# Performance work log

Hardware: AMD Instinct MI355X
Metric: run time of the kernel (lower is better)

Reference implementation:

```python
import jax, jax.numpy as jnp
import numpy as np

NUM_BANDS = 30
SPLIT_FREQ = 30
M_PARAM = 1
DIM = 2048
BATCH = 16384


def _dct_mat(N):
    # Orthonormal DCT-II matrix D: dct(x) = x @ D.T, idct(y) = y @ D
    n = np.arange(N, dtype=np.float64)
    kk = n[:, None]
    M = np.cos(np.pi * (n + 0.5) * kk / N)
    s = np.full(N, np.sqrt(2.0 / N))
    s[0] = np.sqrt(1.0 / N)
    return jnp.asarray((M * s[:, None]).astype(np.float32))


def _band_scale(freq_weights, k, N):
    # Precompute the per-frequency scale vector the torch loop applies band-by-band.
    pts = np.linspace(0, N - 1, NUM_BANDS + 1).astype(np.int64)  # torch .long() truncation
    scale = jnp.ones((N,), dtype=freq_weights.dtype)
    for i in range(NUM_BANDS):
        s, e = int(pts[i]), int(pts[i + 1])
        if e <= SPLIT_FREQ:
            f = 1.0 + freq_weights[i] * k * (1.0 - i / NUM_BANDS)
        else:
            f = 1.0 - freq_weights[i] * k * (1.0 - (i - NUM_BANDS // M_PARAM) / NUM_BANDS)
        scale = scale.at[s:e].set(f)  # bands are disjoint; base is 1
    return scale


def setup_inputs() -> dict:
    key = jax.random.key(0)
    ks = jax.random.split(key, 6)
    g = 0.02  # small init like xavier_uniform with gain 0.5
    return {
        "x": jax.random.normal(ks[0], (BATCH, DIM), dtype=jnp.float32),
        "freq_weights": jnp.ones((NUM_BANDS,), dtype=jnp.float32),
        "k": jnp.float32(0.3),
        "W1": jax.random.normal(ks[1], (1024, DIM), dtype=jnp.float32) * g,
        "b1": jnp.zeros((1024,), dtype=jnp.float32),
        "W2": jax.random.normal(ks[2], (512, 1024), dtype=jnp.float32) * g,
        "b2": jnp.zeros((512,), dtype=jnp.float32),
        "Wmu": jax.random.normal(ks[3], (256, 512), dtype=jnp.float32) * g,
        "bmu": jnp.zeros((256,), dtype=jnp.float32),
        "Wlv": jax.random.normal(ks[4], (256, 512), dtype=jnp.float32) * g,
        "blv": jnp.zeros((256,), dtype=jnp.float32),
    }


def reference(x, freq_weights, k, W1, b1, W2, b2, Wmu, bmu, Wlv, blv):
    N = x.shape[-1]
    D = _dct_mat(N)
    # DCT -> per-band reweight -> IDCT, fused as two matmuls and one vector multiply
    xd = (x @ D.T) * _band_scale(freq_weights, k, N)
    xe = xd @ D
    h = jax.nn.relu(xe @ W1.T + b1)
    h = jax.nn.relu(h @ W2.T + b2)
    mu = h @ Wmu.T + bmu
    logvar = h @ Wlv.T + blv
    return (mu, logvar)
```

## Files before the change

kernel.cpp:

```cpp
#include <hip/hip_runtime.h>
#include <hip/hip_bf16.h>
#include <math.h>

#define DIM 2048
#define BATCH 16384

typedef __attribute__((ext_vector_type(8))) short short8;
typedef __attribute__((ext_vector_type(4))) float floatx4;
typedef unsigned short ushort_t;
typedef unsigned int uint_t;

__device__ __forceinline__ ushort_t f2bf(float f) {
    union { float f; unsigned u; } v; v.f = f;
    unsigned r = v.u + 0x7FFFu + ((v.u >> 16) & 1u);
    return (ushort_t)(r >> 16);
}

__device__ __forceinline__ uint_t cvt2bf(float a, float b) {
    __hip_bfloat162 h = __float22bfloat162_rn(float2{a, b});
    union { __hip_bfloat162 h; uint_t u; } v; v.h = h;
    return v.u;
}

__global__ void k_scale(const float* __restrict__ fw, const float* __restrict__ kp,
                        float* __restrict__ s) {
    int n = blockIdx.x * blockDim.x + threadIdx.x;
    if (n >= DIM) return;
    float kv = kp[0];
    float f = 1.0f;
    for (int i = 0; i < 30; ++i) {
        long s0 = (long)((double)i       * (double)(DIM - 1) / 30.0);
        long e0 = (long)((double)(i + 1) * (double)(DIM - 1) / 30.0);
        if (n >= s0 && n < e0) {
            if (e0 <= 30)
                f = 1.0f + fw[i] * kv * (1.0f - (float)i / 30.0f);
            else
                f = 1.0f - fw[i] * kv * (1.0f - (float)(i - 30) / 30.0f);
        }
    }
    s[n] = f;
}

__global__ void k_gen_d(ushort_t* __restrict__ D, ushort_t* __restrict__ Dt) {
    int idx = blockIdx.x * blockDim.x + threadIdx.x;
    int r = idx >> 11;
    int c = idx & (DIM - 1);
    const float w  = 7.6699039394282058e-4f;
    const float s0 = 0.02209708691207961f;
    const float s1 = 0.03125f;
    int m1 = ((2 * c + 1) * r) & (4 * DIM - 1);
    int m2 = ((2 * r + 1) * c) & (4 * DIM - 1);
    float v1 = cosf(w * (float)m1) * (r == 0 ? s0 : s1);
    float v2 = cosf(w * (float)m2) * (c == 0 ? s0 : s1);
    D[idx]  = f2bf(v1);
    Dt[idx] = f2bf(v2);
}

#define U_W1   262144
#define U_W2    65536
#define U_WH    16384
__global__ void k_cast_w(const float* __restrict__ W1, const float* __restrict__ W2,
                         const float* __restrict__ Wmu, const float* __restrict__ Wlv,
                         ushort_t* __restrict__ W1bf, ushort_t* __restrict__ W2bf,
                         ushort_t* __restrict__ Wcat) {
    int i = blockIdx.x * blockDim.x + threadIdx.x;
    const float* src; ushort_t* dst; int u;
    if (i < U_W1)                    { src = W1;  dst = W1bf;             u = i; }
    else if (i < U_W1 + U_W2)        { src = W2;  dst = W2bf;             u = i - U_W1; }
    else if (i < U_W1 + U_W2 + U_WH) { src = Wmu; dst = Wcat;             u = i - U_W1 - U_W2; }
    else                             { src = Wlv; dst = Wcat + 8 * U_WH;  u = i - U_W1 - U_W2 - U_WH; }
    const float4* p = reinterpret_cast<const float4*>(src) + 2 * (size_t)u;
    float4 a = p[0], b = p[1];
    short8 r;
    r[0] = (short)f2bf(a.x); r[1] = (short)f2bf(a.y);
    r[2] = (short)f2bf(a.z); r[3] = (short)f2bf(a.w);
    r[4] = (short)f2bf(b.x); r[5] = (short)f2bf(b.y);
    r[6] = (short)f2bf(b.z); r[7] = (short)f2bf(b.w);
    *reinterpret_cast<short8*>(dst + 8 * (size_t)u) = r;
}

template<int TM, int TN, int EPI, bool AF32>
__device__ __forceinline__ void gemm_core(
        const ushort_t* __restrict__ A, const float* __restrict__ Af,
        const ushort_t* __restrict__ B,
        ushort_t* __restrict__ Cb, float* __restrict__ Cf,
        const float* __restrict__ ep0, const float* __restrict__ ep1,
        int M, int N, int K) {
    constexpr int BM = 32 * TM;
    constexpr int BN = 32 * TN;
    __shared__ __align__(16) ushort_t As[BM * 32];
    __shared__ __align__(16) ushort_t Bs[BN * 32];

    const int tid  = threadIdx.x;
    const int lane = tid & 63;
    const int wave = tid >> 6;
    const int wm   = wave >> 1;
    const int wn   = wave & 1;
    const int q    = lane >> 4;
    const int l16  = lane & 15;

    const int tilesM = M / BM;
    const int tilesN = N / BN;
    const int bid = (int)blockIdx.x;
    const int xcd = bid & 7;
    const int j   = bid >> 3;
    const int bm  = xcd * (tilesM >> 3) + j / tilesN;
    const int bn  = j % tilesN;

    floatx4 acc[TM][TN];
    #pragma unroll
    for (int i = 0; i < TM; ++i)
        #pragma unroll
        for (int jj = 0; jj < TN; ++jj)
            acc[i][jj] = (floatx4){0.f, 0.f, 0.f, 0.f};

    const long aBase = (long)bm * BM * K;
    const long bBase = (long)bn * BN * K;

    float4 pf[4];
    const float* abase = nullptr;
    if constexpr (AF32) {
        abase = Af + aBase + (long)(tid >> 3) * K + (tid & 7) * 4;
        #pragma unroll
        for (int i = 0; i < 4; ++i)
            pf[i] = *reinterpret_cast<const float4*>(abase + (long)i * 32 * K);
    }

    for (int kt = 0; kt < K; kt += 32) {
        __syncthreads();
        if constexpr (AF32) {
            const int rowb = tid >> 3, fseg = tid & 7;
            #pragma unroll
            for (int i = 0; i < 4; ++i) {
                int row  = rowb + i * 32;
                int lseg = (fseg >> 1) ^ ((row >> 1) & 3);
                uint2 w;
                w.x = cvt2bf(pf[i].x, pf[i].y);
                w.y = cvt2bf(pf[i].z, pf[i].w);
                *reinterpret_cast<uint2*>(As + row * 32 + lseg * 8 + (fseg & 1) * 4) = w;
            }
        } else {
            #pragma unroll
            for (int i = 0; i < BM / 64; ++i) {
                int idx = tid + i * 256;
                int row = idx >> 2, seg = idx & 3;
                int gseg = seg ^ ((row >> 1) & 3);
                const ushort_t* g = A + aBase + (long)row * K + kt + gseg * 8;
                __builtin_amdgcn_global_load_lds(
                    (const __attribute__((address_space(1))) void*)g,
                    (__attribute__((address_space(3))) void*)(As + idx * 8),
                    16, 0, 0);
            }
        }
        #pragma unroll
        for (int i = 0; i < BN / 64; ++i) {
            int idx = tid + i * 256;
            int row = idx >> 2, seg = idx & 3;
            int gseg = seg ^ ((row >> 1) & 3);
            const ushort_t* g = B + bBase + (long)row * K + kt + gseg * 8;
            __builtin_amdgcn_global_load_lds(
                (const __attribute__((address_space(1))) void*)g,
                (__attribute__((address_space(3))) void*)(Bs + idx * 8),
                16, 0, 0);
        }
        __syncthreads();

        short8 af[TM], bfr[TN];
        #pragma unroll
        for (int t = 0; t < TM; ++t) {
            int srow = wm * TM * 16 + t * 16 + l16;
            int rseg = q ^ ((srow >> 1) & 3);
            af[t] = *reinterpret_cast<const short8*>(&As[srow * 32 + rseg * 8]);
        }
        #pragma unroll
        for (int t = 0; t < TN; ++t) {
            int srow = wn * TN * 16 + t * 16 + l16;
            int rseg = q ^ ((srow >> 1) & 3);
            bfr[t] = *reinterpret_cast<const short8*>(&Bs[srow * 32 + rseg * 8]);
        }
        if constexpr (AF32) {
            if (kt + 32 < K) {
                const float* ab = abase + kt + 32;
                #pragma unroll
                for (int i = 0; i < 4; ++i)
                    pf[i] = *reinterpret_cast<const float4*>(ab + (long)i * 32 * K);
            }
        }
        #pragma unroll
        for (int i = 0; i < TM; ++i)
            #pragma unroll
            for (int jj = 0; jj < TN; ++jj)
                acc[i][jj] = __builtin_amdgcn_mfma_f32_16x16x32_bf16(
                    af[i], bfr[jj], acc[i][jj], 0, 0, 0);
    }

    #pragma unroll
    for (int i = 0; i < TM; ++i) {
        #pragma unroll
        for (int jj = 0; jj < TN; ++jj) {
            #pragma unroll
            for (int r = 0; r < 4; ++r) {
                int row = bm * BM + wm * TM * 16 + i * 16 + q * 4 + r;
                int col = bn * BN + wn * TN * 16 + jj * 16 + l16;
                float v = acc[i][jj][r];
                if constexpr (EPI == 0) {
                    Cb[(long)row * N + col] = f2bf(v * ep0[col]);
                } else if constexpr (EPI == 1) {
                    Cb[(long)row * N + col] = f2bf(v);
                } else if constexpr (EPI == 2) {
                    v += ep0[col];
                    v = v > 0.f ? v : 0.f;
                    Cb[(long)row * N + col] = f2bf(v);
                } else {
                    const int half = N >> 1;
                    if (col < half)
                        Cf[(long)row * half + col] = v + ep0[col];
                    else
                        Cf[(long)M * half + (long)row * half + (col - half)] = v + ep1[col - half];
                }
            }
        }
    }
}

__global__ __launch_bounds__(256) void g0_w1d(const ushort_t* A, const ushort_t* B,
        ushort_t* Cb, const float* ep0, int M, int N, int K) {
    gemm_core<2, 2, 0, false>(A, nullptr, B, Cb, nullptr, ep0, nullptr, M, N, K);
}
__global__ __launch_bounds__(256) void g1_m1(const ushort_t* A, const ushort_t* B,
        ushort_t* Cb, int M, int N, int K) {
    gemm_core<2, 2, 1, false>(A, nullptr, B, Cb, nullptr, nullptr, nullptr, M, N, K);
}
__global__ __launch_bounds__(256) void g2_xm1(const float* Af, const ushort_t* B,
        ushort_t* Cb, const float* ep0, int M, int N, int K) {
    gemm_core<4, 4, 2, true>(nullptr, Af, B, Cb, nullptr, ep0, nullptr, M, N, K);
}
__global__ __launch_bounds__(256) void g3_h2(const ushort_t* A, const ushort_t* B,
        ushort_t* Cb, const float* ep0, int M, int N, int K) {
    gemm_core<4, 4, 2, false>(A, nullptr, B, Cb, nullptr, ep0, nullptr, M, N, K);
}
__global__ __launch_bounds__(256) void g4_head(const ushort_t* A, const ushort_t* B,
        float* Cf, const float* ep0, const float* ep1, int M, int N, int K) {
    gemm_core<4, 4, 3, false>(A, nullptr, B, nullptr, Cf, ep0, ep1, M, N, K);
}

extern "C" void kernel_launch(void* const* d_in, const int* in_sizes, int n_in,
                              void* d_out, int out_size, void* d_ws, size_t ws_size,
                              hipStream_t stream) {
    const float* x   = (const float*)d_in[0];
    const float* fw  = (const float*)d_in[1];
    const float* kp  = (const float*)d_in[2];
    const float* W1  = (const float*)d_in[3];
    const float* b1  = (const float*)d_in[4];
    const float* W2  = (const float*)d_in[5];
    const float* b2  = (const float*)d_in[6];
    const float* Wmu = (const float*)d_in[7];
    const float* bmu = (const float*)d_in[8];
    const float* Wlv = (const float*)d_in[9];
    const float* blv = (const float*)d_in[10];
    float* out = (float*)d_out;

    char* ws = (char*)d_ws;
    const size_t MB = 1024 * 1024;
    ushort_t* W1bf = (ushort_t*)(ws + 0);
    ushort_t* Dbf  = (ushort_t*)(ws + 4  * MB);
    ushort_t* Dtbf = (ushort_t*)(ws + 12 * MB);
    ushort_t* T1sT = (ushort_t*)(ws + 20 * MB);
    ushort_t* H1   = (ushort_t*)(ws + 0);
    ushort_t* H2   = (ushort_t*)(ws + 32 * MB);
    ushort_t* M1T  = (ushort_t*)(ws + 48 * MB);
    ushort_t* W2bf = (ushort_t*)(ws + 52 * MB);
    ushort_t* Wcat = (ushort_t*)(ws + 53 * MB);
    float*    svec = (float*)   (ws + 54 * MB);

    hipLaunchKernelGGL(k_scale, dim3(DIM / 256), dim3(256), 0, stream, fw, kp, svec);
    hipLaunchKernelGGL(k_gen_d, dim3(DIM * DIM / 256), dim3(256), 0, stream, Dbf, Dtbf);
    hipLaunchKernelGGL(k_cast_w, dim3((U_W1 + U_W2 + 2 * U_WH) / 256), dim3(256), 0, stream,
                       W1, W2, Wmu, Wlv, W1bf, W2bf, Wcat);

    hipLaunchKernelGGL(g0_w1d, dim3((1024 / 64) * (2048 / 64)), dim3(256), 0, stream,
                       W1bf, Dbf, T1sT, svec, 1024, 2048, 2048);
    hipLaunchKernelGGL(g1_m1, dim3((1024 / 64) * (2048 / 64)), dim3(256), 0, stream,
                       T1sT, Dtbf, M1T, 1024, 2048, 2048);
    hipLaunchKernelGGL(g2_xm1, dim3((BATCH / 128) * (1024 / 128)), dim3(256), 0, stream,
                       x, M1T, H1, b1, BATCH, 1024, 2048);
    hipLaunchKernelGGL(g3_h2, dim3((BATCH / 128) * (512 / 128)), dim3(256), 0, stream,
                       H1, W2bf, H2, b2, BATCH, 512, 1024);
    hipLaunchKernelGGL(g4_head, dim3((BATCH / 128) * (512 / 128)), dim3(256), 0, stream,
                       H2, Wcat, out, bmu, blv, BATCH, 512, 512);

    (void)in_sizes; (void)n_in; (void)out_size; (void)ws_size;
}
```

Before: 455.2 us.

## Load A operand directly into registers, bypassing LDS, for 128-row GEMMs

```diff
diff --git a/kernel.cpp b/kernel.cpp
--- a/kernel.cpp
+++ b/kernel.cpp
@@ -50,8 +50,8 @@
     const float s1 = 0.03125f;
     int m1 = ((2 * c + 1) * r) & (4 * DIM - 1);
     int m2 = ((2 * r + 1) * c) & (4 * DIM - 1);
-    float v1 = cosf(w * (float)m1) * (r == 0 ? s0 : s1);
-    float v2 = cosf(w * (float)m2) * (c == 0 ? s0 : s1);
+    float v1 = __cosf(w * (float)m1) * (r == 0 ? s0 : s1);
+    float v2 = __cosf(w * (float)m2) * (c == 0 ? s0 : s1);
     D[idx]  = f2bf(v1);
     Dt[idx] = f2bf(v2);
 }
@@ -79,7 +79,7 @@
     *reinterpret_cast<short8*>(dst + 8 * (size_t)u) = r;
 }
 
-template<int TM, int TN, int EPI, bool AF32>
+template<int TM, int TN, int EPI, int AMODE>
 __device__ __forceinline__ void gemm_core(
         const ushort_t* __restrict__ A, const float* __restrict__ Af,
         const ushort_t* __restrict__ B,
@@ -88,7 +88,7 @@
         int M, int N, int K) {
     constexpr int BM = 32 * TM;
     constexpr int BN = 32 * TN;
-    __shared__ __align__(16) ushort_t As[BM * 32];
+    __shared__ __align__(16) ushort_t As[(AMODE == 0) ? BM * 32 : 4];
     __shared__ __align__(16) ushort_t Bs[BN * 32];
 
     const int tid  = threadIdx.x;
@@ -117,29 +117,14 @@
     const long aBase = (long)bm * BM * K;
     const long bBase = (long)bn * BN * K;
 
-    float4 pf[4];
-    const float* abase = nullptr;
-    if constexpr (AF32) {
-        abase = Af + aBase + (long)(tid >> 3) * K + (tid & 7) * 4;
-        #pragma unroll
-        for (int i = 0; i < 4; ++i)
-            pf[i] = *reinterpret_cast<const float4*>(abase + (long)i * 32 * K);
-    }
+    const float*    apf = nullptr;
+    const ushort_t* aph = nullptr;
+    if constexpr (AMODE == 1) apf = Af + aBase + (long)(wm * TM * 16 + l16) * K + q * 8;
+    if constexpr (AMODE == 2) aph = A  + aBase + (long)(wm * TM * 16 + l16) * K + q * 8;
 
     for (int kt = 0; kt < K; kt += 32) {
         __syncthreads();
-        if constexpr (AF32) {
-            const int rowb = tid >> 3, fseg = tid & 7;
-            #pragma unroll
-            for (int i = 0; i < 4; ++i) {
-                int row  = rowb + i * 32;
-                int lseg = (fseg >> 1) ^ ((row >> 1) & 3);
-                uint2 w;
-                w.x = cvt2bf(pf[i].x, pf[i].y);
-                w.y = cvt2bf(pf[i].z, pf[i].w);
-                *reinterpret_cast<uint2*>(As + row * 32 + lseg * 8 + (fseg & 1) * 4) = w;
-            }
-        } else {
+        if constexpr (AMODE == 0) {
             #pragma unroll
             for (int i = 0; i < BM / 64; ++i) {
                 int idx = tid + i * 256;
@@ -163,28 +148,51 @@
                 (__attribute__((address_space(3))) void*)(Bs + idx * 8),
                 16, 0, 0);
         }
+        float4 fa[TM], fb[TM];
+        short8 afd[TM];
+        if constexpr (AMODE == 1) {
+            #pragma unroll
+            for (int t = 0; t < TM; ++t) {
+                const float* p = apf + (long)t * 16 * K + kt;
+                fa[t] = *reinterpret_cast<const float4*>(p);
+                fb[t] = *reinterpret_cast<const float4*>(p + 4);
+            }
+        } else if constexpr (AMODE == 2) {
+            #pragma unroll
+            for (int t = 0; t < TM; ++t)
+                afd[t] = *reinterpret_cast<const short8*>(aph + (long)t * 16 * K + kt);
+        }
         __syncthreads();
 
         short8 af[TM], bfr[TN];
-        #pragma unroll
-        for (int t = 0; t < TM; ++t) {
-            int srow = wm * TM * 16 + t * 16 + l16;
-            int rseg = q ^ ((srow >> 1) & 3);
-            af[t] = *reinterpret_cast<const short8*>(&As[srow * 32 + rseg * 8]);
+        if constexpr (AMODE == 0) {
+            #pragma unroll
+            for (int t = 0; t < TM; ++t) {
+                int srow = wm * TM * 16 + t * 16 + l16;
+                int rseg = q ^ ((srow >> 1) & 3);
+                af[t] = *reinterpret_cast<const short8*>(&As[srow * 32 + rseg * 8]);
+            }
+        } else if constexpr (AMODE == 1) {
+            #pragma unroll
+            for (int t = 0; t < TM; ++t) {
+                uint_t w0 = cvt2bf(fa[t].x, fa[t].y);
+                uint_t w1 = cvt2bf(fa[t].z, fa[t].w);
+                uint_t w2 = cvt2bf(fb[t].x, fb[t].y);
+                uint_t w3 = cvt2bf(fb[t].z, fb[t].w);
+                af[t][0] = (short)(w0 & 0xFFFF); af[t][1] = (short)(w0 >> 16);
+                af[t][2] = (short)(w1 & 0xFFFF); af[t][3] = (short)(w1 >> 16);
+                af[t][4] = (short)(w2 & 0xFFFF); af[t][5] = (short)(w2 >> 16);
+                af[t][6] = (short)(w3 & 0xFFFF); af[t][7] = (short)(w3 >> 16);
+            }
+        } else {
+            #pragma unroll
+            for (int t = 0; t < TM; ++t) af[t] = afd[t];
         }
         #pragma unroll
         for (int t = 0; t < TN; ++t) {
             int srow = wn * TN * 16 + t * 16 + l16;
             int rseg = q ^ ((srow >> 1) & 3);
             bfr[t] = *reinterpret_cast<const short8*>(&Bs[srow * 32 + rseg * 8]);
-        }
-        if constexpr (AF32) {
-            if (kt + 32 < K) {
-                const float* ab = abase + kt + 32;
-                #pragma unroll
-                for (int i = 0; i < 4; ++i)
-                    pf[i] = *reinterpret_cast<const float4*>(ab + (long)i * 32 * K);
-            }
         }
         #pragma unroll
         for (int i = 0; i < TM; ++i)
@@ -225,23 +233,23 @@
 
 __global__ __launch_bounds__(256) void g0_w1d(const ushort_t* A, const ushort_t* B,
         ushort_t* Cb, const float* ep0, int M, int N, int K) {
-    gemm_core<2, 2, 0, false>(A, nullptr, B, Cb, nullptr, ep0, nullptr, M, N, K);
+    gemm_core<2, 2, 0, 0>(A, nullptr, B, Cb, nullptr, ep0, nullptr, M, N, K);
 }
 __global__ __launch_bounds__(256) void g1_m1(const ushort_t* A, const ushort_t* B,
         ushort_t* Cb, int M, int N, int K) {
-    gemm_core<2, 2, 1, false>(A, nullptr, B, Cb, nullptr, nullptr, nullptr, M, N, K);
+    gemm_core<2, 2, 1, 0>(A, nullptr, B, Cb, nullptr, nullptr, nullptr, M, N, K);
 }
 __global__ __launch_bounds__(256) void g2_xm1(const float* Af, const ushort_t* B,
         ushort_t* Cb, const float* ep0, int M, int N, int K) {
-    gemm_core<4, 4, 2, true>(nullptr, Af, B, Cb, nullptr, ep0, nullptr, M, N, K);
+    gemm_core<4, 4, 2, 1>(nullptr, Af, B, Cb, nullptr, ep0, nullptr, M, N, K);
 }
 __global__ __launch_bounds__(256) void g3_h2(const ushort_t* A, const ushort_t* B,
         ushort_t* Cb, const float* ep0, int M, int N, int K) {
-    gemm_core<4, 4, 2, false>(A, nullptr, B, Cb, nullptr, ep0, nullptr, M, N, K);
+    gemm_core<4, 4, 2, 2>(A, nullptr, B, Cb, nullptr, ep0, nullptr, M, N, K);
 }
 __global__ __launch_bounds__(256) void g4_head(const ushort_t* A, const ushort_t* B,
         float* Cf, const float* ep0, const float* ep1, int M, int N, int K) {
-    gemm_core<4, 4, 3, false>(A, nullptr, B, nullptr, Cf, ep0, ep1, M, N, K);
+    gemm_core<4, 4, 3, 2>(A, nullptr, B, nullptr, Cf, ep0, ep1, M, N, K);
 }
 
 extern "C" void kernel_launch(void* const* d_in, const int* in_sizes, int n_in,
```

Result: slower. 588.4 us (+29.3%).
